# Kernel optimization log

Hardware: AMD Instinct MI355X
Metric: run time of the kernel (lower is better)

Reference implementation:

```python
import jax, jax.numpy as jnp
import numpy as np
from jax import lax

K = 3          # kernel_size
STRIDE = 1
PAD = 1
DIL = 1


def conv2d(x, w, b):
    y = lax.conv_general_dilated(
        x, w, (STRIDE, STRIDE), [(PAD, PAD), (PAD, PAD)],
        rhs_dilation=(DIL, DIL),
        dimension_numbers=('NCHW', 'OIHW', 'NCHW'))
    return y + b[None, :, None, None]


def setup_inputs() -> dict:
    key = jax.random.key(0)
    ks = jax.random.split(key, 6)
    N, Cin, Cout, H, W = 4, 64, 64, 192, 192
    K2 = K * K
    x_input = jax.random.normal(ks[0], (N, Cin, H, W), jnp.float32)
    # offset branch: 2*K2 output channels (dy, dx per kernel tap); small init
    w_off = jax.random.normal(ks[1], (2 * K2, Cin, K, K), jnp.float32) * 0.01
    b_off = jnp.zeros((2 * K2,), jnp.float32)
    # modulation branch (DCNv2): K2 channels, 2*sigmoid
    w_mod = jax.random.normal(ks[2], (K2, Cin, K, K), jnp.float32) * 0.01
    b_mod = jnp.zeros((K2,), jnp.float32)
    # main conv weight + bias
    w = jax.random.normal(ks[3], (Cout, Cin, K, K), jnp.float32) / np.sqrt(Cin * K2)
    b = jax.random.normal(ks[4], (Cout,), jnp.float32) * 0.01
    return {'x_input': x_input, 'w_off': w_off, 'b_off': b_off,
            'w_mod': w_mod, 'b_mod': b_mod, 'w': w, 'b': b}


def _deform_sample(x, py, px):
    # x [N,C,H,W]; py,px [N,K2,Ho,Wo] -> bilinear samples [N,C,K2,Ho,Wo]
    N, C, H, W = x.shape
    xf = x.reshape(N, C, H * W)
    y0 = jnp.floor(py)
    x0 = jnp.floor(px)
    ly = py - y0
    lx = px - x0
    y0i = y0.astype(jnp.int32)
    x0i = x0.astype(jnp.int32)

    def gather(yi, xi, wt):
        valid = (yi >= 0) & (yi < H) & (xi >= 0) & (xi < W)  # zero padding outside
        idx = jnp.clip(yi, 0, H - 1) * W + jnp.clip(xi, 0, W - 1)
        idx_flat = idx.reshape(N, -1)
        vals = jax.vmap(lambda a, i: jnp.take(a, i, axis=1))(xf, idx_flat)  # [N,C,K2*Ho*Wo]
        vals = vals.reshape(N, C, *yi.shape[1:])
        return vals * (wt * valid)[:, None]

    out = gather(y0i, x0i, (1 - ly) * (1 - lx))
    out = out + gather(y0i, x0i + 1, (1 - ly) * lx)
    out = out + gather(y0i + 1, x0i, ly * (1 - lx))
    out = out + gather(y0i + 1, x0i + 1, ly * lx)
    return out


def reference(x_input, w_off, b_off, w_mod, b_mod, w, b):
    N, C, H, W = x_input.shape
    K2 = K * K
    off = conv2d(x_input, w_off, b_off)                       # [N,2*K2,Ho,Wo]
    mod = 2.0 * jax.nn.sigmoid(conv2d(x_input, w_mod, b_mod))  # [N,K2,Ho,Wo]
    Ho, Wo = off.shape[2], off.shape[3]
    off = off.reshape(N, K2, 2, Ho, Wo)
    ky = jnp.repeat(jnp.arange(K) * DIL, K).astype(jnp.float32)  # [K2]
    kx = jnp.tile(jnp.arange(K) * DIL, K).astype(jnp.float32)
    hy = (jnp.arange(Ho) * STRIDE - PAD).astype(jnp.float32)
    wx = (jnp.arange(Wo) * STRIDE - PAD).astype(jnp.float32)
    py = off[:, :, 0] + hy[None, None, :, None] + ky[None, :, None, None]  # [N,K2,Ho,Wo]
    px = off[:, :, 1] + wx[None, None, None, :] + kx[None, :, None, None]
    val = _deform_sample(x_input, py, px) * mod[:, None]       # [N,C,K2,Ho,Wo]
    out = jnp.einsum('nckhw,ock->nohw', val, w.reshape(w.shape[0], C, K2))
    out = out + b[None, :, None, None]
    return jax.nn.relu(out)
```

## Files before the change

### kernel.cpp

```cpp
#include <hip/hip_runtime.h>
#include <hip/hip_bf16.h>
#include <hip/hip_fp16.h>
#include <math.h>


#define NB   4
#define CIN  64
#define COUT 64
#define HH   192
#define WW   192
#define HW   (HH*WW)

typedef __attribute__((ext_vector_type(4))) float f32x4;
typedef __attribute__((ext_vector_type(8))) _Float16 f16x8;
typedef __attribute__((ext_vector_type(4))) unsigned int u32x4;
typedef __attribute__((ext_vector_type(4))) int i32x4;

__device__ __forceinline__ int iclamp(int v, int lo, int hi) {
    return v < lo ? lo : (v > hi ? hi : v);
}
__device__ __forceinline__ unsigned short f16bits(float f) {
    __half h = __float2half(f);
    union { __half h; unsigned short u; } t; t.h = h; return t.u;
}
__device__ __forceinline__ float h2f(unsigned short u) {
    union { unsigned short u; __half h; } t; t.u = u; return __half2float(t.h);
}
__device__ __forceinline__ unsigned int dup16(float f) {
    unsigned int b = f16bits(f);
    return b | (b << 16);
}

__global__ __launch_bounds__(256) void to_nhwc(
        const float* __restrict__ x, unsigned short* __restrict__ xt) {
    int n  = blockIdx.y;
    int px = blockIdx.x * 256 + threadIdx.x;
    const float* xn = x + (size_t)n * CIN * HW + px;
    union { unsigned short us[64]; u32x4 q[8]; } pk;
#pragma unroll
    for (int c = 0; c < 64; c++) pk.us[c] = f16bits(xn[c * HW]);
    u32x4* dst = (u32x4*)(xt + ((size_t)n * HW + px) * 64);
#pragma unroll
    for (int i = 0; i < 8; i++) dst[i] = pk.q[i];
}

__global__ __launch_bounds__(256) void prep_weights(
        const float* __restrict__ w, const float* __restrict__ w_off,
        const float* __restrict__ w_mod, const float* __restrict__ b_off,
        const float* __restrict__ b_mod, unsigned short* __restrict__ wfrag,
        unsigned short* __restrict__ wauxf, float* __restrict__ baux) {
    int idx = blockIdx.x * 256 + threadIdx.x;
    if (idx < 36864) {
        int j    = idx & 7;
        int lane = (idx >> 3) & 63;
        int kc   = (idx >> 9) & 1;
        int g    = (idx >> 10) & 3;
        int k    = idx >> 12;
        int o = g * 16 + (lane & 15);
        int c = kc * 32 + (lane >> 4) * 8 + j;
        wfrag[idx] = f16bits(w[(o * 64 + c) * 9 + k]);
    }
    if (idx < 18432) {
        int j    = idx & 7;
        int lane = (idx >> 3) & 63;
        int kc   = (idx >> 9) & 1;
        int ga   = (idx >> 10) & 1;
        int k    = idx >> 11;
        int o = ga * 16 + (lane & 15);
        int c = kc * 32 + (lane >> 4) * 8 + j;
        float v = 0.f;
        if (o < 18)      v = w_off[(o * 64 + c) * 9 + k];
        else if (o < 27) v = w_mod[((o - 18) * 64 + c) * 9 + k];
        wauxf[idx] = f16bits(v);
    }
    if (idx < 32) {
        float v = 0.f;
        if (idx < 18)      v = b_off[idx];
        else if (idx < 27) v = b_mod[idx - 18];
        baux[idx] = v;
    }
}

__global__ __launch_bounds__(256, 3) void dcn_fused(
        const unsigned short* __restrict__ xt,
        const unsigned short* __restrict__ wfrag,
        const unsigned short* __restrict__ wauxf,
        const float* __restrict__ baux,
        const float* __restrict__ bias,
        float* __restrict__ out) {
    __shared__ __align__(16) unsigned short win[216 * 64];
    __shared__ __align__(16) unsigned short oml[2][32][32];
    __shared__ __align__(16) u32x4 planW[576];
    __shared__ __align__(16) i32x4 planC[576];

    int tid = threadIdx.x;
    int l   = tid & 63;
    int wv  = __builtin_amdgcn_readfirstlane(tid >> 6);
    int r2  = wv >> 1;
    int g2  = wv & 1;

    int id = blockIdx.x;
    int sw = (id & 7) * 288 + (id >> 3);
    int n  = sw / 576;
    int r  = sw % 576;
    int ho2    = (r / 6) * 2;
    int wobase = (r % 6) * 32;

    const char* xb = (const char*)xt + (size_t)n * HW * 128;

    if (tid < 216) {
        int rw = tid / 36, cl = tid - rw * 36;
        int gy = iclamp(ho2 - 2 + rw, 0, HH - 1);
        int gx = iclamp(wobase - 2 + cl, 0, WW - 1);
        const u32x4* src = (const u32x4*)(xb + ((size_t)gy * WW + gx) * 128);
        char* dst = (char*)win + tid * 128;
        int xw = (tid & 7) << 4;
#pragma unroll
        for (int c = 0; c < 8; c++)
            *(u32x4*)(dst + ((c * 16) ^ xw)) = src[c];
    }
    __syncthreads();

    {
        f32x4 aacc[2];
        aacc[0] = (f32x4){0.f, 0.f, 0.f, 0.f};
        aacc[1] = (f32x4){0.f, 0.f, 0.f, 0.f};
        const f16x8 zero8 = (f16x8){0, 0, 0, 0, 0, 0, 0, 0};
        int pa   = g2 * 16 + (l & 15);
        int cba  = (l >> 4) * 16;
        int ho_a = ho2 + r2;

#pragma unroll 1
        for (int k = 0; k < 9; k++) {
            int ky = k / 3, kx = k - 3 * (k / 3);
            int ys = ho_a + ky - 1;
            if ((unsigned)ys >= (unsigned)HH) continue;
            int xs = wobase + pa + kx - 1;
            bool ok = (unsigned)xs < (unsigned)WW;
            int sA = (ky + 1 + r2) * 36 + (pa + kx + 1);
            const char* pp = (const char*)win + sA * 128;
            int xw = (sA & 7) << 4;
            const f16x8* wa = ((const f16x8*)wauxf) + (k * 4) * 64 + l;
#pragma unroll
            for (int kc = 0; kc < 2; kc++) {
                f16x8 bv = *(const f16x8*)(pp + ((kc * 64 + cba) ^ xw));
                if (!ok) bv = zero8;
                f16x8 a0 = wa[(kc)     * 64];
                f16x8 a1 = wa[(2 + kc) * 64];
                aacc[0] = __builtin_amdgcn_mfma_f32_16x16x32_f16(a0, bv, aacc[0], 0, 0, 0);
                aacc[1] = __builtin_amdgcn_mfma_f32_16x16x32_f16(a1, bv, aacc[1], 0, 0, 0);
            }
        }
#pragma unroll
        for (int h = 0; h < 2; h++) {
#pragma unroll
            for (int rr = 0; rr < 2; rr++) {
                int o = h * 16 + (l >> 4) * 4 + rr * 2;
                float v0 = aacc[h][rr * 2]     + baux[o];
                float v1 = aacc[h][rr * 2 + 1] + baux[o + 1];
                if (o     >= 18) v0 = 2.f / (1.f + expf(-v0));
                if (o + 1 >= 18) v1 = 2.f / (1.f + expf(-v1));
                unsigned int pk = (unsigned int)f16bits(v0)
                                | ((unsigned int)f16bits(v1) << 16);
                *(unsigned int*)&oml[r2][pa][o] = pk;
            }
        }
    }
    __syncthreads();

    for (int i = tid; i < 576; i += 256) {
        int rp = i / 9;
        int k  = i - rp * 9;
        int r2p = rp >> 5, px = rp & 31;
        int ho_p  = ho2 + r2p;
        int wox_p = wobase + px;

        int ky = k / 3, kx = k - 3 * (k / 3);
        unsigned int oyx = *(const unsigned int*)&oml[r2p][px][2 * k];
        float offy = h2f((unsigned short)(oyx & 0xffffu));
        float offx = h2f((unsigned short)(oyx >> 16));
        float mm   = h2f(oml[r2p][px][18 + k]);
        float py  = offy + (float)(ho_p - 1 + ky);
        float pxf = offx + (float)(wox_p - 1 + kx);
        float y0f = floorf(py), x0f = floorf(pxf);
        float ly = py - y0f, lx = pxf - x0f;
        int y0 = (int)y0f, x0 = (int)x0f;
        int y1 = y0 + 1, x1 = x0 + 1;
        bool y0ok = (unsigned)y0 < (unsigned)HH, y1ok = (unsigned)y1 < (unsigned)HH;
        bool x0ok = (unsigned)x0 < (unsigned)WW, x1ok = (unsigned)x1 < (unsigned)WW;
        float wt0 = (y0ok && x0ok) ? mm * (1.f - ly) * (1.f - lx) : 0.f;
        float wt1 = (y0ok && x1ok) ? mm * (1.f - ly) * lx         : 0.f;
        float wt2 = (y1ok && x0ok) ? mm * ly * (1.f - lx)         : 0.f;
        float wt3 = (y1ok && x1ok) ? mm * ly * lx                 : 0.f;
        int y0c = iclamp(y0, 0, HH - 1), y1c = iclamp(y1, 0, HH - 1);
        int x0c = iclamp(x0, 0, WW - 1), x1c = iclamp(x1, 0, WW - 1);
        int sy0 = y0c - ho2 + 2,    sy1 = y1c - ho2 + 2;
        int sx0 = x0c - wobase + 2, sx1 = x1c - wobase + 2;
        int sy0c = iclamp(sy0, 0, 5),  sy1c = iclamp(sy1, 0, 5);
        int sx0c = iclamp(sx0, 0, 35), sx1c = iclamp(sx1, 0, 35);
        bool fb0 = (wt0 > 0.f) && ((sy0 != sy0c) | (sx0 != sx0c));
        bool fb1 = (wt1 > 0.f) && ((sy0 != sy0c) | (sx1 != sx1c));
        bool fb2 = (wt2 > 0.f) && ((sy1 != sy1c) | (sx0 != sx0c));
        bool fb3 = (wt3 > 0.f) && ((sy1 != sy1c) | (sx1 != sx1c));
        int c0 = fb0 ? -(y0c * WW + x0c) - 1 : sy0c * 36 + sx0c;
        int c1 = fb1 ? -(y0c * WW + x1c) - 1 : sy0c * 36 + sx1c;
        int c2 = fb2 ? -(y1c * WW + x0c) - 1 : sy1c * 36 + sx0c;
        int c3 = fb3 ? -(y1c * WW + x1c) - 1 : sy1c * 36 + sx1c;

        planW[i] = (u32x4){dup16(wt0), dup16(wt1), dup16(wt2), dup16(wt3)};
        planC[i] = (i32x4){c0, c1, c2, c3};
    }
    __syncthreads();

    f32x4 acc[4];
#pragma unroll
    for (int nf = 0; nf < 4; nf++) acc[nf] = (f32x4){0.f, 0.f, 0.f, 0.f};

    int p_loc = l & 15;
    int chunk = l >> 4;
    int p     = g2 * 16 + p_loc;
    int ho_w  = ho2 + r2;
    int cb0   = chunk * 16;
    int cb1   = cb0 + 64;
    const char* planWp = (const char*)planW + (r2 * 32 + p) * 9 * 16;
    const char* planCp = (const char*)planC + (r2 * 32 + p) * 9 * 16;

    union Q { u32x4 u; __half2 h2[4]; };

#pragma unroll 1
    for (int k = 0; k < 9; k++) {
        const f16x8* wfk = ((const f16x8*)wfrag) + (k * 8) * 64 + l;
        f16x8 wB[8];
#pragma unroll
        for (int f = 0; f < 8; f++) wB[f] = wfk[f * 64];

        union { u32x4 u; __half2 h2[4]; } pw;
        pw.u = *(const u32x4*)(planWp + k * 16);
        i32x4 pc = *(const i32x4*)(planCp + k * 16);
        int c0 = pc.x, c1 = pc.y, c2 = pc.z, c3 = pc.w;

        int d0 = c0 < 0 ? 0 : c0, d1 = c1 < 0 ? 0 : c1;
        int d2 = c2 < 0 ? 0 : c2, d3 = c3 < 0 ? 0 : c3;
        const char* b0 = (const char*)win + d0 * 128;
        const char* b1 = (const char*)win + d1 * 128;
        const char* b2 = (const char*)win + d2 * 128;
        const char* b3 = (const char*)win + d3 * 128;
        int x0 = (d0 & 7) << 4, x1 = (d1 & 7) << 4;
        int x2 = (d2 & 7) << 4, x3 = (d3 & 7) << 4;
        Q q0, q1, q2, q3, q4, q5, q6, q7;
        q0.u = *(const u32x4*)(b0 + (cb0 ^ x0));
        q1.u = *(const u32x4*)(b0 + (cb1 ^ x0));
        q2.u = *(const u32x4*)(b1 + (cb0 ^ x1));
        q3.u = *(const u32x4*)(b1 + (cb1 ^ x1));
        q4.u = *(const u32x4*)(b2 + (cb0 ^ x2));
        q5.u = *(const u32x4*)(b2 + (cb1 ^ x2));
        q6.u = *(const u32x4*)(b3 + (cb0 ^ x3));
        q7.u = *(const u32x4*)(b3 + (cb1 ^ x3));

        if (__builtin_expect((c0 | c1 | c2 | c3) < 0, 0)) {
            if (c0 < 0) { const char* gp = xb + (size_t)(-c0 - 1) * 128 + cb0;
                          q0.u = *(const u32x4*)gp; q1.u = *(const u32x4*)(gp + 64); }
            if (c1 < 0) { const char* gp = xb + (size_t)(-c1 - 1) * 128 + cb0;
                          q2.u = *(const u32x4*)gp; q3.u = *(const u32x4*)(gp + 64); }
            if (c2 < 0) { const char* gp = xb + (size_t)(-c2 - 1) * 128 + cb0;
                          q4.u = *(const u32x4*)gp; q5.u = *(const u32x4*)(gp + 64); }
            if (c3 < 0) { const char* gp = xb + (size_t)(-c3 - 1) * 128 + cb0;
                          q6.u = *(const u32x4*)gp; q7.u = *(const u32x4*)(gp + 64); }
        }

        union { __half2 h2[4]; f16x8 v; } fA0, fA1;
#pragma unroll
        for (int j = 0; j < 4; j++) {
            __half2 t = __hmul2(q0.h2[j], pw.h2[0]);
            t = __hfma2(q2.h2[j], pw.h2[1], t);
            t = __hfma2(q4.h2[j], pw.h2[2], t);
            t = __hfma2(q6.h2[j], pw.h2[3], t);
            fA0.h2[j] = t;
            __half2 s = __hmul2(q1.h2[j], pw.h2[0]);
            s = __hfma2(q3.h2[j], pw.h2[1], s);
            s = __hfma2(q5.h2[j], pw.h2[2], s);
            s = __hfma2(q7.h2[j], pw.h2[3], s);
            fA1.h2[j] = s;
        }

        __builtin_amdgcn_s_setprio(1);
#pragma unroll
        for (int nf = 0; nf < 4; nf++) {
            acc[nf] = __builtin_amdgcn_mfma_f32_16x16x32_f16(fA0.v, wB[nf * 2],     acc[nf], 0, 0, 0);
            acc[nf] = __builtin_amdgcn_mfma_f32_16x16x32_f16(fA1.v, wB[nf * 2 + 1], acc[nf], 0, 0, 0);
        }
        __builtin_amdgcn_s_setprio(0);
    }

#pragma unroll
    for (int nf = 0; nf < 4; nf++) {
        int o = nf * 16 + p_loc;
        float bo = bias[o];
        int wo = wobase + g2 * 16 + chunk * 4;
        float* op = out + (((size_t)n * COUT + o) * HH + ho_w) * WW + wo;
#pragma unroll
        for (int rr = 0; rr < 4; rr++) {
            float v = acc[nf][rr] + bo;
            op[rr] = fmaxf(v, 0.f);
        }
    }
}

extern "C" void kernel_launch(void* const* d_in, const int* in_sizes, int n_in,
                              void* d_out, int out_size, void* d_ws, size_t ws_size,
                              hipStream_t stream) {
    const float* x     = (const float*)d_in[0];
    const float* w_off = (const float*)d_in[1];
    const float* b_off = (const float*)d_in[2];
    const float* w_mod = (const float*)d_in[3];
    const float* b_mod = (const float*)d_in[4];
    const float* w     = (const float*)d_in[5];
    const float* b     = (const float*)d_in[6];
    float* out = (float*)d_out;

    unsigned short* wfrag = (unsigned short*)d_ws;
    unsigned short* wauxf = wfrag + 36864;
    float* baux = (float*)(wauxf + 18432);
    unsigned short* xt = (unsigned short*)(baux + 32);

    to_nhwc<<<dim3(144, NB), dim3(256), 0, stream>>>(x, xt);
    prep_weights<<<dim3(144), dim3(256), 0, stream>>>(w, w_off, w_mod, b_off,
                                                      b_mod, wfrag, wauxf, baux);
    dcn_fused<<<dim3(2304), dim3(256), 0, stream>>>(xt, wfrag, wauxf, baux, b, out);
}
```

Before: 72.43 us.

## Pack sampling plan into one 16-byte LDS entry and raise occupancy to 4

```diff
diff --git a/kernel.cpp b/kernel.cpp
--- a/kernel.cpp
+++ b/kernel.cpp
@@ -14,7 +14,6 @@
 typedef __attribute__((ext_vector_type(4))) float f32x4;
 typedef __attribute__((ext_vector_type(8))) _Float16 f16x8;
 typedef __attribute__((ext_vector_type(4))) unsigned int u32x4;
-typedef __attribute__((ext_vector_type(4))) int i32x4;
 
 __device__ __forceinline__ int iclamp(int v, int lo, int hi) {
     return v < lo ? lo : (v > hi ? hi : v);
@@ -26,9 +25,15 @@
 __device__ __forceinline__ float h2f(unsigned short u) {
     union { unsigned short u; __half h; } t; t.u = u; return __half2float(t.h);
 }
-__device__ __forceinline__ unsigned int dup16(float f) {
-    unsigned int b = f16bits(f);
-    return b | (b << 16);
+__device__ __forceinline__ __half2 dup_lo(unsigned int u) {
+    unsigned int lo = u & 0xffffu;
+    unsigned int d = lo | (lo << 16);
+    union { unsigned int u; __half2 h; } t; t.u = d; return t.h;
+}
+__device__ __forceinline__ __half2 dup_hi(unsigned int u) {
+    unsigned int hi = u >> 16;
+    unsigned int d = hi | (hi << 16);
+    union { unsigned int u; __half2 h; } t; t.u = d; return t.h;
 }
 
 __global__ __launch_bounds__(256) void to_nhwc(
@@ -81,7 +86,7 @@
     }
 }
 
-__global__ __launch_bounds__(256, 3) void dcn_fused(
+__global__ __launch_bounds__(256, 4) void dcn_fused(
         const unsigned short* __restrict__ xt,
         const unsigned short* __restrict__ wfrag,
         const unsigned short* __restrict__ wauxf,
@@ -90,8 +95,7 @@
         float* __restrict__ out) {
     __shared__ __align__(16) unsigned short win[216 * 64];
     __shared__ __align__(16) unsigned short oml[2][32][32];
-    __shared__ __align__(16) u32x4 planW[576];
-    __shared__ __align__(16) i32x4 planC[576];
+    __shared__ __align__(16) u32x4 plan[576];
 
     int tid = threadIdx.x;
     int l   = tid & 63;
@@ -202,13 +206,14 @@
         bool fb1 = (wt1 > 0.f) && ((sy0 != sy0c) | (sx1 != sx1c));
         bool fb2 = (wt2 > 0.f) && ((sy1 != sy1c) | (sx0 != sx0c));
         bool fb3 = (wt3 > 0.f) && ((sy1 != sy1c) | (sx1 != sx1c));
-        int c0 = fb0 ? -(y0c * WW + x0c) - 1 : sy0c * 36 + sx0c;
-        int c1 = fb1 ? -(y0c * WW + x1c) - 1 : sy0c * 36 + sx1c;
-        int c2 = fb2 ? -(y1c * WW + x0c) - 1 : sy1c * 36 + sx0c;
-        int c3 = fb3 ? -(y1c * WW + x1c) - 1 : sy1c * 36 + sx1c;
-
-        planW[i] = (u32x4){dup16(wt0), dup16(wt1), dup16(wt2), dup16(wt3)};
-        planC[i] = (i32x4){c0, c1, c2, c3};
+        unsigned int c0 = fb0 ? 0xffffu : (unsigned int)(sy0c * 36 + sx0c);
+        unsigned int c1 = fb1 ? 0xffffu : (unsigned int)(sy0c * 36 + sx1c);
+        unsigned int c2 = fb2 ? 0xffffu : (unsigned int)(sy1c * 36 + sx0c);
+        unsigned int c3 = fb3 ? 0xffffu : (unsigned int)(sy1c * 36 + sx1c);
+
+        unsigned int w01 = (unsigned int)f16bits(wt0) | ((unsigned int)f16bits(wt1) << 16);
+        unsigned int w23 = (unsigned int)f16bits(wt2) | ((unsigned int)f16bits(wt3) << 16);
+        plan[i] = (u32x4){w01, w23, c0 | (c1 << 16), c2 | (c3 << 16)};
     }
     __syncthreads();
 
@@ -220,10 +225,11 @@
     int chunk = l >> 4;
     int p     = g2 * 16 + p_loc;
     int ho_w  = ho2 + r2;
+    int wox   = wobase + p;
     int cb0   = chunk * 16;
     int cb1   = cb0 + 64;
-    const char* planWp = (const char*)planW + (r2 * 32 + p) * 9 * 16;
-    const char* planCp = (const char*)planC + (r2 * 32 + p) * 9 * 16;
+    const u32x4* plp = plan + (r2 * 32 + p) * 9;
+    const unsigned short* omp = &oml[r2][p][0];
 
     union Q { u32x4 u; __half2 h2[4]; };
 
@@ -234,13 +240,12 @@
 #pragma unroll
         for (int f = 0; f < 8; f++) wB[f] = wfk[f * 64];
 
-        union { u32x4 u; __half2 h2[4]; } pw;
-        pw.u = *(const u32x4*)(planWp + k * 16);
-        i32x4 pc = *(const i32x4*)(planCp + k * 16);
-        int c0 = pc.x, c1 = pc.y, c2 = pc.z, c3 = pc.w;
-
-        int d0 = c0 < 0 ? 0 : c0, d1 = c1 < 0 ? 0 : c1;
-        int d2 = c2 < 0 ? 0 : c2, d3 = c3 < 0 ? 0 : c3;
+        u32x4 pl = plp[k];
+        unsigned int c0 = pl.z & 0xffffu, c1 = pl.z >> 16;
+        unsigned int c2 = pl.w & 0xffffu, c3 = pl.w >> 16;
+
+        int d0 = (int)(c0 & 255u), d1 = (int)(c1 & 255u);
+        int d2 = (int)(c2 & 255u), d3 = (int)(c3 & 255u);
         const char* b0 = (const char*)win + d0 * 128;
         const char* b1 = (const char*)win + d1 * 128;
         const char* b2 = (const char*)win + d2 * 128;
@@ -257,29 +262,41 @@
         q6.u = *(const u32x4*)(b3 + (cb0 ^ x3));
         q7.u = *(const u32x4*)(b3 + (cb1 ^ x3));
 
-        if (__builtin_expect((c0 | c1 | c2 | c3) < 0, 0)) {
-            if (c0 < 0) { const char* gp = xb + (size_t)(-c0 - 1) * 128 + cb0;
-                          q0.u = *(const u32x4*)gp; q1.u = *(const u32x4*)(gp + 64); }
-            if (c1 < 0) { const char* gp = xb + (size_t)(-c1 - 1) * 128 + cb0;
-                          q2.u = *(const u32x4*)gp; q3.u = *(const u32x4*)(gp + 64); }
-            if (c2 < 0) { const char* gp = xb + (size_t)(-c2 - 1) * 128 + cb0;
-                          q4.u = *(const u32x4*)gp; q5.u = *(const u32x4*)(gp + 64); }
-            if (c3 < 0) { const char* gp = xb + (size_t)(-c3 - 1) * 128 + cb0;
-                          q6.u = *(const u32x4*)gp; q7.u = *(const u32x4*)(gp + 64); }
-        }
-
+        if (__builtin_expect((c0 == 0xffffu) | (c1 == 0xffffu) |
+                             (c2 == 0xffffu) | (c3 == 0xffffu), 0)) {
+            int ky = k / 3, kx = k - 3 * (k / 3);
+            unsigned int oyx = *(const unsigned int*)(omp + 2 * k);
+            float offy = h2f((unsigned short)(oyx & 0xffffu));
+            float offx = h2f((unsigned short)(oyx >> 16));
+            float py  = offy + (float)(ho_w - 1 + ky);
+            float pxf = offx + (float)(wox - 1 + kx);
+            int y0 = (int)floorf(py), x0i = (int)floorf(pxf);
+            int y0c = iclamp(y0, 0, HH - 1),     y1c = iclamp(y0 + 1, 0, HH - 1);
+            int x0c = iclamp(x0i, 0, WW - 1),    x1c = iclamp(x0i + 1, 0, WW - 1);
+            if (c0 == 0xffffu) { const char* gp = xb + ((size_t)y0c * WW + x0c) * 128 + cb0;
+                                 q0.u = *(const u32x4*)gp; q1.u = *(const u32x4*)(gp + 64); }
+            if (c1 == 0xffffu) { const char* gp = xb + ((size_t)y0c * WW + x1c) * 128 + cb0;
+                                 q2.u = *(const u32x4*)gp; q3.u = *(const u32x4*)(gp + 64); }
+            if (c2 == 0xffffu) { const char* gp = xb + ((size_t)y1c * WW + x0c) * 128 + cb0;
+                                 q4.u = *(const u32x4*)gp; q5.u = *(const u32x4*)(gp + 64); }
+            if (c3 == 0xffffu) { const char* gp = xb + ((size_t)y1c * WW + x1c) * 128 + cb0;
+                                 q6.u = *(const u32x4*)gp; q7.u = *(const u32x4*)(gp + 64); }
+        }
+
+        __half2 wv0 = dup_lo(pl.x), wv1 = dup_hi(pl.x);
+        __half2 wv2 = dup_lo(pl.y), wv3 = dup_hi(pl.y);
         union { __half2 h2[4]; f16x8 v; } fA0, fA1;
 #pragma unroll
         for (int j = 0; j < 4; j++) {
-            __half2 t = __hmul2(q0.h2[j], pw.h2[0]);
-            t = __hfma2(q2.h2[j], pw.h2[1], t);
-            t = __hfma2(q4.h2[j], pw.h2[2], t);
-            t = __hfma2(q6.h2[j], pw.h2[3], t);
+            __half2 t = __hmul2(q0.h2[j], wv0);
+            t = __hfma2(q2.h2[j], wv1, t);
+            t = __hfma2(q4.h2[j], wv2, t);
+            t = __hfma2(q6.h2[j], wv3, t);
             fA0.h2[j] = t;
-            __half2 s = __hmul2(q1.h2[j], pw.h2[0]);
-            s = __hfma2(q3.h2[j], pw.h2[1], s);
-            s = __hfma2(q5.h2[j], pw.h2[2], s);
-            s = __hfma2(q7.h2[j], pw.h2[3], s);
+            __half2 s = __hmul2(q1.h2[j], wv0);
+            s = __hfma2(q3.h2[j], wv1, s);
+            s = __hfma2(q5.h2[j], wv2, s);
+            s = __hfma2(q7.h2[j], wv3, s);
             fA1.h2[j] = s;
         }
 
```

Result: no change. 71.47 us (-1.3%).
